# Kernel tuning notes

Measured on AMD Instinct MI355X. Metric: run time of the kernel, lower is better.

The kernel has to match this reference:

```python
import jax, jax.numpy as jnp
import numpy as np


def setup_inputs() -> dict:
    key = jax.random.key(0)
    k1, k2 = jax.random.split(key)
    sat = jax.random.normal(k1, (32, 64, 64, 64), dtype=jnp.float32)
    grd = jax.random.normal(k2, (32, 64, 64, 64), dtype=jnp.float32)
    return {"sat_features": sat, "grd_features": grd}


def _corr(sat, grd):
    # sat: [Bs,C,H,W], grd: [Bg,C,gh,gw] with H==gh and W==gw (enforced by source asserts)
    Bs, C, H, W = sat.shape
    Bg, _, gh, gw = grd.shape
    n = gw - 1
    # source circularly pads the HEIGHT axis by gw-1 (inner_warp_pad_columns, dim=2)
    satpad = jnp.concatenate([sat, sat[:, :, :n, :]], axis=2)  # [Bs,C,H+gw-1,W]
    # torch conv2d is cross-correlation with kernel = grd flipped along width.
    # Batch all Bs x Bg pairs as one conv: kernels are OIHW with O=Bg.
    kernel = jnp.flip(grd, axis=3)  # [Bg,C,gh,gw]
    out = jax.lax.conv_general_dilated(
        satpad, kernel, window_strides=(1, 1), padding='VALID',
        dimension_numbers=('NCHW', 'OIHW', 'NCHW'))  # [Bs,Bg,gw,1]
    out = out[..., 0]                                # [Bs,Bg,gw] (squeeze(3))
    orien = jnp.argmax(out, axis=2)                  # [Bs,Bg] int
    return out, orien


def _crop_sat(sat, orien, grd_width):
    # Per-pair circular shift along sat WIDTH, then crop first grd_width columns.
    Bs, C, H, W = sat.shape
    Bg = orien.shape[1]
    idx = (jnp.arange(grd_width)[None, None, :] + orien[:, :, None]) % W  # [Bs,Bg,gw]
    sat_e = jnp.broadcast_to(sat[:, None], (Bs, Bg, C, H, W))
    idx_e = jnp.broadcast_to(idx[:, :, None, None, :], (Bs, Bg, C, H, grd_width))
    # cropped[i,j,c,h,k] = sat[i,c,h,(k+orien[i,j]) % W]
    return jnp.take_along_axis(sat_e, idx_e, axis=4)  # [Bs,Bg,C,H,grd_width]


def _forward(sat, grd):
    corr_out, orien = _corr(sat, grd)
    grd_width = grd.shape[2]
    cropped = _crop_sat(sat, orien, grd_width)
    norm = jnp.sqrt(jnp.sum(cropped ** 2, axis=(2, 3, 4), keepdims=True) + 1e-8)
    sat_matrix = cropped / norm
    dot = jnp.sum(sat_matrix * grd[None], axis=(2, 3, 4))  # [Bs,Bg]
    distance = 2.0 - 2.0 * dot.T                           # [Bg,Bs]
    return distance, orien


def reference(sat_features, grd_features):
    distance, orien = _forward(sat_features, grd_features)
    return (sat_features, grd_features, distance, orien)
```

## Files before the change

### kernel.cpp

```cpp
#include <hip/hip_runtime.h>

typedef _Float16 f16;
typedef _Float16 f16x8 __attribute__((ext_vector_type(8)));
typedef float f32x16 __attribute__((ext_vector_type(16)));

#define SAT_ELEMS (32*64*64*64)
#define PER_I (64*64*64)
#define DIST_OFF (2*SAT_ELEMS)
#define ORIEN_OFF (DIST_OFF + 32*32)

#define WS_NORMS 0
#define WS_ORIEN 64
#define WS_CORR  2048
#define WS_DOTS  67584

__global__ __launch_bounds__(256) void zero_kernel(float* __restrict__ ws) {
  int t = blockIdx.x * 256 + threadIdx.x;
  if (t < 65536 + 1024) ws[WS_CORR + t] = 0.f;
}

__global__ __launch_bounds__(256) void copy_kernel(const float4* __restrict__ sat,
                                                   const float4* __restrict__ grd,
                                                   float4* __restrict__ out) {
  const int n4 = SAT_ELEMS / 4;
  int idx = blockIdx.x * 256 + threadIdx.x;
  int stride = gridDim.x * 256;
  for (int t = idx; t < n4; t += stride) out[t] = sat[t];
  for (int t = idx; t < n4; t += stride) out[n4 + t] = grd[t];
}

__global__ __launch_bounds__(256) void norm_kernel(const float4* __restrict__ sat,
                                                   float* __restrict__ norms) {
  int i = blockIdx.x;
  const float4* p = sat + (size_t)i * (PER_I / 4);
  float s = 0.f;
  for (int t = threadIdx.x; t < PER_I / 4; t += 256) {
    float4 v = p[t];
    s += v.x * v.x + v.y * v.y + v.z * v.z + v.w * v.w;
  }
  for (int off = 32; off; off >>= 1) s += __shfl_down(s, off, 64);
  __shared__ float red[4];
  int lane = threadIdx.x & 63, wv = threadIdx.x >> 6;
  if (lane == 0) red[wv] = s;
  __syncthreads();
  if (threadIdx.x == 0) norms[i] = sqrtf(red[0] + red[1] + red[2] + red[3] + 1e-8f);
}

__global__ __launch_bounds__(512) void gram3_kernel(const float* __restrict__ sat,
                                                    const float* __restrict__ grd,
                                                    float* __restrict__ ws) {
  __shared__ f16 As[2][256][64];
  __shared__ f16 Bs[2][128][64];
  __shared__ float corr_s[8][64];

  const int bid = blockIdx.x;
  const int ipg = bid & 7;
  const int rem = bid >> 3;
  const int jpg = rem >> 2;
  const int kz  = rem & 3;

  const int tid = threadIdx.x;
  const int lane = tid & 63;
  const int wv = tid >> 6;
  const int wr = wv >> 1, wc = wv & 1;
  const int lr = lane & 31, lh = lane >> 5;

  const int ra = tid >> 1, ua = tid & 1;
  const int ia = ipg * 4 + (ra >> 6), ha = ra & 63;
  const bool hasB = (tid < 256);
  const int rb = (tid >> 1) & 127, ub = tid & 1;
  const int jb = jpg * 2 + (rb >> 6), hb = rb & 63;

  const float* abase = sat + (size_t)ia * PER_I + (size_t)ha * 64;
  const float* bbase = grd + (size_t)jb * PER_I + (size_t)hb * 64;

  f32x16 acc[2][2];
  #pragma unroll
  for (int mh = 0; mh < 2; ++mh)
    #pragma unroll
    for (int nh = 0; nh < 2; ++nh)
      #pragma unroll
      for (int q = 0; q < 16; ++q) acc[mh][nh][q] = 0.f;

  float4 avA[4], avB[4];

  auto LOADA = [&](int S) {
    const int c = S >> 1, w0 = (S & 1) * 32;
    const float* p = abase + (size_t)c * 4096 + w0 + ua * 16;
    #pragma unroll
    for (int q = 0; q < 4; ++q) avA[q] = *(const float4*)(p + q * 4);
  };
  auto LOADB = [&](int S) {
    const int c = S >> 1, w0 = (S & 1) * 32;
    const float* p = bbase + (size_t)c * 4096;
    #pragma unroll
    for (int q = 0; q < 4; ++q) avB[q] = *(const float4*)(p + 60 - w0 - ub * 16 - q * 4);
  };
  auto WRITEA = [&](int buf) {
    f16* row = &As[buf][ra][0];
    const int rx = ra & 7;
    #pragma unroll
    for (int half = 0; half < 2; ++half) {
      f16x8 h, l;
      #pragma unroll
      for (int q = 0; q < 2; ++q) {
        float4 v = avA[half * 2 + q];
        const float xs[4] = {v.x, v.y, v.z, v.w};
        #pragma unroll
        for (int e = 0; e < 4; ++e) {
          f16 hh = (f16)xs[e];
          h[q * 4 + e] = hh;
          l[q * 4 + e] = (f16)(xs[e] - (float)hh);
        }
      }
      const int ck = 2 * ua + half;
      *(f16x8*)(row + ((ck ^ rx) * 8)) = h;
      *(f16x8*)(row + (((ck + 4) ^ rx) * 8)) = l;
    }
  };
  auto WRITEB = [&](int buf) {
    f16* row = &Bs[buf][rb][0];
    const int rx = rb & 7;
    #pragma unroll
    for (int half = 0; half < 2; ++half) {
      f16x8 h, l;
      #pragma unroll
      for (int q = 0; q < 2; ++q) {
        float4 v = avB[half * 2 + q];
        const float xs[4] = {v.w, v.z, v.y, v.x};
        #pragma unroll
        for (int e = 0; e < 4; ++e) {
          f16 hh = (f16)xs[e];
          h[q * 4 + e] = hh;
          l[q * 4 + e] = (f16)(xs[e] - (float)hh);
        }
      }
      const int ck = 2 * ub + half;
      *(f16x8*)(row + ((ck ^ rx) * 8)) = h;
      *(f16x8*)(row + (((ck + 4) ^ rx) * 8)) = l;
    }
  };

  const int aro = wr * 64, bro = wc * 64;
  const int S0 = kz * 32;

  LOADA(S0); if (hasB) LOADB(S0);
  WRITEA(0); if (hasB) WRITEB(0);
  __syncthreads();

  int cur = 0;
  for (int s = 0; s < 32; ++s) {
    if (s < 31) { LOADA(S0 + s + 1); if (hasB) LOADB(S0 + s + 1); }
    #pragma unroll
    for (int kk = 0; kk < 2; ++kk) {
      f16x8 ah[2], al[2], bh[2], bl[2];
      const int c0 = kk * 2 + lh;
      #pragma unroll
      for (int mh = 0; mh < 2; ++mh) {
        const int r1 = aro + mh * 32 + lr, rk1 = r1 & 7;
        ah[mh] = *(const f16x8*)(&As[cur][r1][0] + ((c0 ^ rk1) * 8));
        al[mh] = *(const f16x8*)(&As[cur][r1][0] + (((c0 + 4) ^ rk1) * 8));
        const int r2 = bro + mh * 32 + lr, rk2 = r2 & 7;
        bh[mh] = *(const f16x8*)(&Bs[cur][r2][0] + ((c0 ^ rk2) * 8));
        bl[mh] = *(const f16x8*)(&Bs[cur][r2][0] + (((c0 + 4) ^ rk2) * 8));
      }
      #pragma unroll
      for (int mh = 0; mh < 2; ++mh)
        #pragma unroll
        for (int nh = 0; nh < 2; ++nh) {
          acc[mh][nh] = __builtin_amdgcn_mfma_f32_32x32x16_f16(ah[mh], bh[nh], acc[mh][nh], 0, 0, 0);
          acc[mh][nh] = __builtin_amdgcn_mfma_f32_32x32x16_f16(ah[mh], bl[nh], acc[mh][nh], 0, 0, 0);
          acc[mh][nh] = __builtin_amdgcn_mfma_f32_32x32x16_f16(al[mh], bh[nh], acc[mh][nh], 0, 0, 0);
        }
    }
    if (s < 31) { WRITEA(cur ^ 1); if (hasB) WRITEB(cur ^ 1); }
    __syncthreads();
    cur ^= 1;
  }

  ((float*)corr_s)[tid] = 0.f;
  __syncthreads();
  const int p = wr * 2 + wc;
  #pragma unroll
  for (int r = 0; r < 16; ++r) {
    const int rowof = (r & 3) + 8 * (r >> 2);
    const int y0 = (rowof + 4 * lh - lr) & 63;
    const int y1 = (y0 + 32) & 63;
    atomicAdd(&corr_s[p][y0], acc[0][0][r] + acc[1][1][r]);
    atomicAdd(&corr_s[p][y1], acc[0][1][r] + acc[1][0][r]);
  }
  __syncthreads();
  {
    const int pp = tid >> 6, y = tid & 63;
    const int ip = ipg * 4 + (pp >> 1), jp = jpg * 2 + (pp & 1);
    atomicAdd(&ws[WS_CORR + ((size_t)ip * 32 + jp) * 64 + y], corr_s[pp][y]);
  }
}

__global__ __launch_bounds__(256) void argmax_kernel(const float* __restrict__ ws,
                                                     float* __restrict__ out,
                                                     int* __restrict__ orien) {
  int p = blockIdx.x * 256 + threadIdx.x;
  if (p >= 1024) return;
  const float* c = ws + WS_CORR + (size_t)p * 64;
  float best = c[0];
  int by = 0;
  for (int y = 1; y < 64; ++y) {
    float v = c[y];
    if (v > best) { best = v; by = y; }
  }
  orien[p] = by;
  out[ORIEN_OFF + p] = (float)by;
}

__global__ __launch_bounds__(512) void dot3_kernel(const float* __restrict__ sat,
                                                   const float* __restrict__ grd,
                                                   const int* __restrict__ orien,
                                                   float* __restrict__ dots) {
  const int bi = blockIdx.x;
  const int bj = blockIdx.y;
  const int bz = blockIdx.z;
  const int tid = threadIdx.x, lane = tid & 63, wvj = tid >> 6;
  const int j = bj * 8 + wvj;
  const int r0 = bz * 256;
  const int i0 = bi * 8;
  const float* gp = grd + (size_t)j * PER_I + (size_t)r0 * 64 + lane;
  const float* sp[8];
  #pragma unroll
  for (int q = 0; q < 8; ++q)
    sp[q] = sat + (size_t)(i0 + q) * PER_I + (size_t)r0 * 64
                + ((lane + orien[(i0 + q) * 32 + j]) & 63);
  float a[8] = {0.f, 0.f, 0.f, 0.f, 0.f, 0.f, 0.f, 0.f};
  #pragma unroll 2
  for (int r = 0; r < 256; ++r) {
    float g = gp[(size_t)r * 64];
    #pragma unroll
    for (int q = 0; q < 8; ++q) a[q] = fmaf(sp[q][(size_t)r * 64], g, a[q]);
  }
  #pragma unroll
  for (int q = 0; q < 8; ++q) {
    float s = a[q];
    for (int off = 32; off; off >>= 1) s += __shfl_down(s, off, 64);
    if (lane == 0) atomicAdd(&dots[(i0 + q) * 32 + j], s);
  }
}

__global__ __launch_bounds__(256) void finalize_kernel(const float* __restrict__ ws,
                                                       float* __restrict__ out) {
  int t = blockIdx.x * 256 + threadIdx.x;
  if (t >= 1024) return;
  int jj = t >> 5, ii = t & 31;
  float dot = ws[WS_DOTS + ii * 32 + jj] / ws[WS_NORMS + ii];
  out[DIST_OFF + jj * 32 + ii] = 2.f - 2.f * dot;
}

extern "C" void kernel_launch(void* const* d_in, const int* in_sizes, int n_in,
                              void* d_out, int out_size, void* d_ws, size_t ws_size,
                              hipStream_t stream) {
  const float* sat = (const float*)d_in[0];
  const float* grd = (const float*)d_in[1];
  float* out = (float*)d_out;
  float* wsf = (float*)d_ws;

  zero_kernel<<<260, 256, 0, stream>>>(wsf);
  copy_kernel<<<2048, 256, 0, stream>>>((const float4*)sat, (const float4*)grd, (float4*)out);
  norm_kernel<<<32, 256, 0, stream>>>((const float4*)sat, wsf + WS_NORMS);
  gram3_kernel<<<512, 512, 0, stream>>>(sat, grd, wsf);
  argmax_kernel<<<4, 256, 0, stream>>>(wsf, out, (int*)(wsf + WS_ORIEN));
  dot3_kernel<<<dim3(4, 4, 16), 512, 0, stream>>>(sat, grd, (const int*)(wsf + WS_ORIEN), wsf + WS_DOTS);
  finalize_kernel<<<4, 256, 0, stream>>>(wsf, out);
}
```

Before: 409.9 us.

## Pre-split inputs to fp16 hi/lo in workspace and stream via global_load_lds

Adds a split pass that converts sat and a width-flipped grd into fp16 high and low halves stored in workspace. A new correlation kernel with 256 threads, 128x128 tiles and K split in two loads these directly into LDS with global_load_lds, removing per-block fp32 loads and conversion. The dot-product kernel now reads only the fp16 high parts, halving its bytes at some precision cost. The new path runs only if the workspace is large enough, otherwise it falls back to the old kernels. The split pass adds a full extra read and write of both inputs.

```diff
diff --git a/kernel.cpp b/kernel.cpp
--- a/kernel.cpp
+++ b/kernel.cpp
@@ -1,4 +1,5 @@
 #include <hip/hip_runtime.h>
+#include <stdint.h>
 
 typedef _Float16 f16;
 typedef _Float16 f16x8 __attribute__((ext_vector_type(8)));
@@ -13,6 +14,17 @@
 #define WS_ORIEN 64
 #define WS_CORR  2048
 #define WS_DOTS  67584
+#define WSB_SATH (1u<<20)
+#define WSB_SATL (WSB_SATH + (uint32_t)SAT_ELEMS*2u)
+#define WSB_GRDH (WSB_SATL + (uint32_t)SAT_ELEMS*2u)
+#define WSB_GRDL (WSB_GRDH + (uint32_t)SAT_ELEMS*2u)
+#define WS_NEED  ((size_t)WSB_GRDL + (size_t)SAT_ELEMS*2u + 1024u)
+
+__device__ __forceinline__ void gll16(const void* src, void* dst) {
+  __builtin_amdgcn_global_load_lds(
+      (const __attribute__((address_space(1))) uint32_t*)src,
+      (__attribute__((address_space(3))) uint32_t*)dst, 16, 0, 0);
+}
 
 __global__ __launch_bounds__(256) void zero_kernel(float* __restrict__ ws) {
   int t = blockIdx.x * 256 + threadIdx.x;
@@ -46,33 +58,81 @@
   if (threadIdx.x == 0) norms[i] = sqrtf(red[0] + red[1] + red[2] + red[3] + 1e-8f);
 }
 
-__global__ __launch_bounds__(512) void gram3_kernel(const float* __restrict__ sat,
+__global__ __launch_bounds__(256) void split_kernel(const float* __restrict__ sat,
                                                     const float* __restrict__ grd,
-                                                    float* __restrict__ ws) {
-  __shared__ f16 As[2][256][64];
+                                                    uint8_t* __restrict__ wsb) {
+  f16* satH = (f16*)(wsb + WSB_SATH);
+  f16* satL = (f16*)(wsb + WSB_SATL);
+  f16* grdH = (f16*)(wsb + WSB_GRDH);
+  f16* grdL = (f16*)(wsb + WSB_GRDL);
+  const int NG = SAT_ELEMS / 8;
+  int idx = blockIdx.x * 256 + threadIdx.x;
+  int stride = gridDim.x * 256;
+  for (int g = idx; g < NG; g += stride) {
+    {
+      float4 f0 = *(const float4*)(sat + (size_t)g * 8);
+      float4 f1 = *(const float4*)(sat + (size_t)g * 8 + 4);
+      const float xs[8] = {f0.x, f0.y, f0.z, f0.w, f1.x, f1.y, f1.z, f1.w};
+      f16x8 h, l;
+      #pragma unroll
+      for (int e = 0; e < 8; ++e) {
+        f16 hh = (f16)xs[e];
+        h[e] = hh;
+        l[e] = (f16)(xs[e] - (float)hh);
+      }
+      *(f16x8*)(satH + (size_t)g * 8) = h;
+      *(f16x8*)(satL + (size_t)g * 8) = l;
+    }
+    {
+      int rowg = g >> 3, t = g & 7;
+      const float* gsrc = grd + (size_t)rowg * 64 + (56 - 8 * t);
+      float4 g0 = *(const float4*)(gsrc);
+      float4 g1 = *(const float4*)(gsrc + 4);
+      const float ys[8] = {g1.w, g1.z, g1.y, g1.x, g0.w, g0.z, g0.y, g0.x};
+      f16x8 h, l;
+      #pragma unroll
+      for (int e = 0; e < 8; ++e) {
+        f16 hh = (f16)ys[e];
+        h[e] = hh;
+        l[e] = (f16)(ys[e] - (float)hh);
+      }
+      *(f16x8*)(grdH + (size_t)g * 8) = h;
+      *(f16x8*)(grdL + (size_t)g * 8) = l;
+    }
+  }
+}
+
+__global__ __launch_bounds__(256, 2) void gram4_kernel(const uint8_t* __restrict__ wsb,
+                                                       float* __restrict__ ws) {
+  __shared__ f16 As[2][128][64];
   __shared__ f16 Bs[2][128][64];
-  __shared__ float corr_s[8][64];
+  __shared__ float corr_s[4][64];
 
   const int bid = blockIdx.x;
-  const int ipg = bid & 7;
-  const int rem = bid >> 3;
-  const int jpg = rem >> 2;
-  const int kz  = rem & 3;
-
-  const int tid = threadIdx.x;
-  const int lane = tid & 63;
-  const int wv = tid >> 6;
+  const int wg = (bid & 7) * 64 + (bid >> 3);
+  const int ipg = wg >> 5;
+  const int rem = wg & 31;
+  const int jpg = rem >> 1;
+  const int kz = rem & 1;
+
+  const int tid = threadIdx.x, lane = tid & 63, wv = tid >> 6;
   const int wr = wv >> 1, wc = wv & 1;
   const int lr = lane & 31, lh = lane >> 5;
 
-  const int ra = tid >> 1, ua = tid & 1;
-  const int ia = ipg * 4 + (ra >> 6), ha = ra & 63;
-  const bool hasB = (tid < 256);
-  const int rb = (tid >> 1) & 127, ub = tid & 1;
-  const int jb = jpg * 2 + (rb >> 6), hb = rb & 63;
-
-  const float* abase = sat + (size_t)ia * PER_I + (size_t)ha * 64;
-  const float* bbase = grd + (size_t)jb * PER_I + (size_t)hb * 64;
+  const int rsub = lane >> 3;
+  const int ck = (lane & 7) ^ rsub;
+  uint32_t aoff[4], boff[4];
+  #pragma unroll
+  for (int q = 0; q < 4; ++q) {
+    const int cc = wv * 4 + q;
+    const int row = cc * 8 + rsub;
+    const int h = row & 63, sub = row >> 6;
+    const uint32_t lanepart = 2u * ((uint32_t)h * 64u + (uint32_t)(ck & 3) * 8u);
+    aoff[q] = (ck < 4 ? WSB_SATH : WSB_SATL)
+            + 2u * (uint32_t)(ipg * 2 + sub) * (uint32_t)PER_I + lanepart;
+    boff[q] = (ck < 4 ? WSB_GRDH : WSB_GRDL)
+            + 2u * (uint32_t)(jpg * 2 + sub) * (uint32_t)PER_I + lanepart;
+  }
 
   f32x16 acc[2][2];
   #pragma unroll
@@ -82,85 +142,33 @@
       #pragma unroll
       for (int q = 0; q < 16; ++q) acc[mh][nh][q] = 0.f;
 
-  float4 avA[4], avB[4];
-
-  auto LOADA = [&](int S) {
-    const int c = S >> 1, w0 = (S & 1) * 32;
-    const float* p = abase + (size_t)c * 4096 + w0 + ua * 16;
-    #pragma unroll
-    for (int q = 0; q < 4; ++q) avA[q] = *(const float4*)(p + q * 4);
+  auto ISSUE = [&](int s, int buf) {
+    const int k0 = kz * 2048 + s * 32;
+    const uint32_t so = 2u * ((uint32_t)(k0 >> 6) * 4096u + (uint32_t)(k0 & 63));
+    #pragma unroll
+    for (int q = 0; q < 4; ++q) {
+      const int cc = wv * 4 + q;
+      gll16(wsb + aoff[q] + so, &As[buf][cc * 8][0]);
+      gll16(wsb + boff[q] + so, &Bs[buf][cc * 8][0]);
+    }
   };
-  auto LOADB = [&](int S) {
-    const int c = S >> 1, w0 = (S & 1) * 32;
-    const float* p = bbase + (size_t)c * 4096;
-    #pragma unroll
-    for (int q = 0; q < 4; ++q) avB[q] = *(const float4*)(p + 60 - w0 - ub * 16 - q * 4);
-  };
-  auto WRITEA = [&](int buf) {
-    f16* row = &As[buf][ra][0];
-    const int rx = ra & 7;
-    #pragma unroll
-    for (int half = 0; half < 2; ++half) {
-      f16x8 h, l;
-      #pragma unroll
-      for (int q = 0; q < 2; ++q) {
-        float4 v = avA[half * 2 + q];
-        const float xs[4] = {v.x, v.y, v.z, v.w};
-        #pragma unroll
-        for (int e = 0; e < 4; ++e) {
-          f16 hh = (f16)xs[e];
-          h[q * 4 + e] = hh;
-          l[q * 4 + e] = (f16)(xs[e] - (float)hh);
-        }
-      }
-      const int ck = 2 * ua + half;
-      *(f16x8*)(row + ((ck ^ rx) * 8)) = h;
-      *(f16x8*)(row + (((ck + 4) ^ rx) * 8)) = l;
-    }
-  };
-  auto WRITEB = [&](int buf) {
-    f16* row = &Bs[buf][rb][0];
-    const int rx = rb & 7;
-    #pragma unroll
-    for (int half = 0; half < 2; ++half) {
-      f16x8 h, l;
-      #pragma unroll
-      for (int q = 0; q < 2; ++q) {
-        float4 v = avB[half * 2 + q];
-        const float xs[4] = {v.w, v.z, v.y, v.x};
-        #pragma unroll
-        for (int e = 0; e < 4; ++e) {
-          f16 hh = (f16)xs[e];
-          h[q * 4 + e] = hh;
-          l[q * 4 + e] = (f16)(xs[e] - (float)hh);
-        }
-      }
-      const int ck = 2 * ub + half;
-      *(f16x8*)(row + ((ck ^ rx) * 8)) = h;
-      *(f16x8*)(row + (((ck + 4) ^ rx) * 8)) = l;
-    }
-  };
-
-  const int aro = wr * 64, bro = wc * 64;
-  const int S0 = kz * 32;
-
-  LOADA(S0); if (hasB) LOADB(S0);
-  WRITEA(0); if (hasB) WRITEB(0);
+
+  ISSUE(0, 0);
   __syncthreads();
 
   int cur = 0;
-  for (int s = 0; s < 32; ++s) {
-    if (s < 31) { LOADA(S0 + s + 1); if (hasB) LOADB(S0 + s + 1); }
+  for (int s = 0; s < 64; ++s) {
+    if (s < 63) ISSUE(s + 1, cur ^ 1);
     #pragma unroll
     for (int kk = 0; kk < 2; ++kk) {
       f16x8 ah[2], al[2], bh[2], bl[2];
       const int c0 = kk * 2 + lh;
       #pragma unroll
       for (int mh = 0; mh < 2; ++mh) {
-        const int r1 = aro + mh * 32 + lr, rk1 = r1 & 7;
+        const int r1 = wr * 64 + mh * 32 + lr, rk1 = r1 & 7;
         ah[mh] = *(const f16x8*)(&As[cur][r1][0] + ((c0 ^ rk1) * 8));
         al[mh] = *(const f16x8*)(&As[cur][r1][0] + (((c0 + 4) ^ rk1) * 8));
-        const int r2 = bro + mh * 32 + lr, rk2 = r2 & 7;
+        const int r2 = wc * 64 + mh * 32 + lr, rk2 = r2 & 7;
         bh[mh] = *(const f16x8*)(&Bs[cur][r2][0] + ((c0 ^ rk2) * 8));
         bl[mh] = *(const f16x8*)(&Bs[cur][r2][0] + (((c0 + 4) ^ rk2) * 8));
       }
@@ -173,26 +181,24 @@
           acc[mh][nh] = __builtin_amdgcn_mfma_f32_32x32x16_f16(al[mh], bh[nh], acc[mh][nh], 0, 0, 0);
         }
     }
-    if (s < 31) { WRITEA(cur ^ 1); if (hasB) WRITEB(cur ^ 1); }
     __syncthreads();
     cur ^= 1;
   }
 
-  ((float*)corr_s)[tid] = 0.f;
-  __syncthreads();
-  const int p = wr * 2 + wc;
+  if (tid < 256) ((float*)corr_s)[tid] = 0.f;
+  __syncthreads();
   #pragma unroll
   for (int r = 0; r < 16; ++r) {
     const int rowof = (r & 3) + 8 * (r >> 2);
     const int y0 = (rowof + 4 * lh - lr) & 63;
     const int y1 = (y0 + 32) & 63;
-    atomicAdd(&corr_s[p][y0], acc[0][0][r] + acc[1][1][r]);
-    atomicAdd(&corr_s[p][y1], acc[0][1][r] + acc[1][0][r]);
+    atomicAdd(&corr_s[wv][y0], acc[0][0][r] + acc[1][1][r]);
+    atomicAdd(&corr_s[wv][y1], acc[0][1][r] + acc[1][0][r]);
   }
   __syncthreads();
   {
     const int pp = tid >> 6, y = tid & 63;
-    const int ip = ipg * 4 + (pp >> 1), jp = jpg * 2 + (pp & 1);
+    const int ip = ipg * 2 + (pp >> 1), jp = jpg * 2 + (pp & 1);
     atomicAdd(&ws[WS_CORR + ((size_t)ip * 32 + jp) * 64 + y], corr_s[pp][y]);
   }
 }
@@ -211,6 +217,188 @@
   }
   orien[p] = by;
   out[ORIEN_OFF + p] = (float)by;
+}
+
+__global__ __launch_bounds__(512) void dot4_kernel(const uint8_t* __restrict__ wsb,
+                                                   const int* __restrict__ orien,
+                                                   float* __restrict__ dots) {
+  const f16* satH = (const f16*)(wsb + WSB_SATH);
+  const f16* grdH = (const f16*)(wsb + WSB_GRDH);
+  const int bi = blockIdx.x;
+  const int bj = blockIdx.y;
+  const int bz = blockIdx.z;
+  const int tid = threadIdx.x, lane = tid & 63, wvj = tid >> 6;
+  const int j = bj * 8 + wvj;
+  const int r0 = bz * 256;
+  const int i0 = bi * 8;
+  const f16* gp = grdH + (size_t)j * PER_I + (size_t)r0 * 64 + (63 - lane);
+  const f16* sp[8];
+  #pragma unroll
+  for (int q = 0; q < 8; ++q)
+    sp[q] = satH + (size_t)(i0 + q) * PER_I + (size_t)r0 * 64
+                 + ((lane + orien[(i0 + q) * 32 + j]) & 63);
+  float a[8] = {0.f, 0.f, 0.f, 0.f, 0.f, 0.f, 0.f, 0.f};
+  #pragma unroll 2
+  for (int r = 0; r < 256; ++r) {
+    float g = (float)gp[(size_t)r * 64];
+    #pragma unroll
+    for (int q = 0; q < 8; ++q) a[q] = fmaf((float)sp[q][(size_t)r * 64], g, a[q]);
+  }
+  #pragma unroll
+  for (int q = 0; q < 8; ++q) {
+    float s = a[q];
+    for (int off = 32; off; off >>= 1) s += __shfl_down(s, off, 64);
+    if (lane == 0) atomicAdd(&dots[(i0 + q) * 32 + j], s);
+  }
+}
+
+__global__ __launch_bounds__(256) void finalize_kernel(const float* __restrict__ ws,
+                                                       float* __restrict__ out) {
+  int t = blockIdx.x * 256 + threadIdx.x;
+  if (t >= 1024) return;
+  int jj = t >> 5, ii = t & 31;
+  float dot = ws[WS_DOTS + ii * 32 + jj] / ws[WS_NORMS + ii];
+  out[DIST_OFF + jj * 32 + ii] = 2.f - 2.f * dot;
+}
+
+__global__ __launch_bounds__(512) void gram3_kernel(const float* __restrict__ sat,
+                                                    const float* __restrict__ grd,
+                                                    float* __restrict__ ws) {
+  __shared__ f16 As[2][256][64];
+  __shared__ f16 Bs[2][128][64];
+  __shared__ float corr_s[8][64];
+  const int bid = blockIdx.x;
+  const int ipg = bid & 7;
+  const int rem = bid >> 3;
+  const int jpg = rem >> 2;
+  const int kz  = rem & 3;
+  const int tid = threadIdx.x;
+  const int lane = tid & 63;
+  const int wv = tid >> 6;
+  const int wr = wv >> 1, wc = wv & 1;
+  const int lr = lane & 31, lh = lane >> 5;
+  const int ra = tid >> 1, ua = tid & 1;
+  const int ia = ipg * 4 + (ra >> 6), ha = ra & 63;
+  const bool hasB = (tid < 256);
+  const int rb = (tid >> 1) & 127, ub = tid & 1;
+  const int jb = jpg * 2 + (rb >> 6), hb = rb & 63;
+  const float* abase = sat + (size_t)ia * PER_I + (size_t)ha * 64;
+  const float* bbase = grd + (size_t)jb * PER_I + (size_t)hb * 64;
+  f32x16 acc[2][2];
+  #pragma unroll
+  for (int mh = 0; mh < 2; ++mh)
+    #pragma unroll
+    for (int nh = 0; nh < 2; ++nh)
+      #pragma unroll
+      for (int q = 0; q < 16; ++q) acc[mh][nh][q] = 0.f;
+  float4 avA[4], avB[4];
+  auto LOADA = [&](int S) {
+    const int c = S >> 1, w0 = (S & 1) * 32;
+    const float* p = abase + (size_t)c * 4096 + w0 + ua * 16;
+    #pragma unroll
+    for (int q = 0; q < 4; ++q) avA[q] = *(const float4*)(p + q * 4);
+  };
+  auto LOADB = [&](int S) {
+    const int c = S >> 1, w0 = (S & 1) * 32;
+    const float* p = bbase + (size_t)c * 4096;
+    #pragma unroll
+    for (int q = 0; q < 4; ++q) avB[q] = *(const float4*)(p + 60 - w0 - ub * 16 - q * 4);
+  };
+  auto WRITEA = [&](int buf) {
+    f16* row = &As[buf][ra][0];
+    const int rx = ra & 7;
+    #pragma unroll
+    for (int half = 0; half < 2; ++half) {
+      f16x8 h, l;
+      #pragma unroll
+      for (int q = 0; q < 2; ++q) {
+        float4 v = avA[half * 2 + q];
+        const float xs[4] = {v.x, v.y, v.z, v.w};
+        #pragma unroll
+        for (int e = 0; e < 4; ++e) {
+          f16 hh = (f16)xs[e];
+          h[q * 4 + e] = hh;
+          l[q * 4 + e] = (f16)(xs[e] - (float)hh);
+        }
+      }
+      const int ckk = 2 * ua + half;
+      *(f16x8*)(row + ((ckk ^ rx) * 8)) = h;
+      *(f16x8*)(row + (((ckk + 4) ^ rx) * 8)) = l;
+    }
+  };
+  auto WRITEB = [&](int buf) {
+    f16* row = &Bs[buf][rb][0];
+    const int rx = rb & 7;
+    #pragma unroll
+    for (int half = 0; half < 2; ++half) {
+      f16x8 h, l;
+      #pragma unroll
+      for (int q = 0; q < 2; ++q) {
+        float4 v = avB[half * 2 + q];
+        const float xs[4] = {v.w, v.z, v.y, v.x};
+        #pragma unroll
+        for (int e = 0; e < 4; ++e) {
+          f16 hh = (f16)xs[e];
+          h[q * 4 + e] = hh;
+          l[q * 4 + e] = (f16)(xs[e] - (float)hh);
+        }
+      }
+      const int ckk = 2 * ub + half;
+      *(f16x8*)(row + ((ckk ^ rx) * 8)) = h;
+      *(f16x8*)(row + (((ckk + 4) ^ rx) * 8)) = l;
+    }
+  };
+  const int aro = wr * 64, bro = wc * 64;
+  const int S0 = kz * 32;
+  LOADA(S0); if (hasB) LOADB(S0);
+  WRITEA(0); if (hasB) WRITEB(0);
+  __syncthreads();
+  int cur = 0;
+  for (int s = 0; s < 32; ++s) {
+    if (s < 31) { LOADA(S0 + s + 1); if (hasB) LOADB(S0 + s + 1); }
+    #pragma unroll
+    for (int kk = 0; kk < 2; ++kk) {
+      f16x8 ah[2], al[2], bh[2], bl[2];
+      const int c0 = kk * 2 + lh;
+      #pragma unroll
+      for (int mh = 0; mh < 2; ++mh) {
+        const int r1 = aro + mh * 32 + lr, rk1 = r1 & 7;
+        ah[mh] = *(const f16x8*)(&As[cur][r1][0] + ((c0 ^ rk1) * 8));
+        al[mh] = *(const f16x8*)(&As[cur][r1][0] + (((c0 + 4) ^ rk1) * 8));
+        const int r2 = bro + mh * 32 + lr, rk2 = r2 & 7;
+        bh[mh] = *(const f16x8*)(&Bs[cur][r2][0] + ((c0 ^ rk2) * 8));
+        bl[mh] = *(const f16x8*)(&Bs[cur][r2][0] + (((c0 + 4) ^ rk2) * 8));
+      }
+      #pragma unroll
+      for (int mh = 0; mh < 2; ++mh)
+        #pragma unroll
+        for (int nh = 0; nh < 2; ++nh) {
+          acc[mh][nh] = __builtin_amdgcn_mfma_f32_32x32x16_f16(ah[mh], bh[nh], acc[mh][nh], 0, 0, 0);
+          acc[mh][nh] = __builtin_amdgcn_mfma_f32_32x32x16_f16(ah[mh], bl[nh], acc[mh][nh], 0, 0, 0);
+          acc[mh][nh] = __builtin_amdgcn_mfma_f32_32x32x16_f16(al[mh], bh[nh], acc[mh][nh], 0, 0, 0);
+        }
+    }
+    if (s < 31) { WRITEA(cur ^ 1); if (hasB) WRITEB(cur ^ 1); }
+    __syncthreads();
+    cur ^= 1;
+  }
+  ((float*)corr_s)[tid] = 0.f;
+  __syncthreads();
+  const int p = wr * 2 + wc;
+  #pragma unroll
+  for (int r = 0; r < 16; ++r) {
+    const int rowof = (r & 3) + 8 * (r >> 2);
+    const int y0 = (rowof + 4 * lh - lr) & 63;
+    const int y1 = (y0 + 32) & 63;
+    atomicAdd(&corr_s[p][y0], acc[0][0][r] + acc[1][1][r]);
+    atomicAdd(&corr_s[p][y1], acc[0][1][r] + acc[1][0][r]);
+  }
+  __syncthreads();
+  {
+    const int pp = tid >> 6, y = tid & 63;
+    const int ip = ipg * 4 + (pp >> 1), jp = jpg * 2 + (pp & 1);
+    atomicAdd(&ws[WS_CORR + ((size_t)ip * 32 + jp) * 64 + y], corr_s[pp][y]);
+  }
 }
 
 __global__ __launch_bounds__(512) void dot3_kernel(const float* __restrict__ sat,
@@ -245,15 +433,6 @@
   }
 }
 
-__global__ __launch_bounds__(256) void finalize_kernel(const float* __restrict__ ws,
-                                                       float* __restrict__ out) {
-  int t = blockIdx.x * 256 + threadIdx.x;
-  if (t >= 1024) return;
-  int jj = t >> 5, ii = t & 31;
-  float dot = ws[WS_DOTS + ii * 32 + jj] / ws[WS_NORMS + ii];
-  out[DIST_OFF + jj * 32 + ii] = 2.f - 2.f * dot;
-}
-
 extern "C" void kernel_launch(void* const* d_in, const int* in_sizes, int n_in,
                               void* d_out, int out_size, void* d_ws, size_t ws_size,
                               hipStream_t stream) {
@@ -261,12 +440,21 @@
   const float* grd = (const float*)d_in[1];
   float* out = (float*)d_out;
   float* wsf = (float*)d_ws;
+  uint8_t* wsb = (uint8_t*)d_ws;
 
   zero_kernel<<<260, 256, 0, stream>>>(wsf);
   copy_kernel<<<2048, 256, 0, stream>>>((const float4*)sat, (const float4*)grd, (float4*)out);
   norm_kernel<<<32, 256, 0, stream>>>((const float4*)sat, wsf + WS_NORMS);
-  gram3_kernel<<<512, 512, 0, stream>>>(sat, grd, wsf);
-  argmax_kernel<<<4, 256, 0, stream>>>(wsf, out, (int*)(wsf + WS_ORIEN));
-  dot3_kernel<<<dim3(4, 4, 16), 512, 0, stream>>>(sat, grd, (const int*)(wsf + WS_ORIEN), wsf + WS_DOTS);
+
+  if (ws_size >= WS_NEED) {
+    split_kernel<<<2048, 256, 0, stream>>>(sat, grd, wsb);
+    gram4_kernel<<<512, 256, 0, stream>>>(wsb, wsf);
+    argmax_kernel<<<4, 256, 0, stream>>>(wsf, out, (int*)(wsf + WS_ORIEN));
+    dot4_kernel<<<dim3(4, 4, 16), 512, 0, stream>>>(wsb, (const int*)(wsf + WS_ORIEN), wsf + WS_DOTS);
+  } else {
+    gram3_kernel<<<512, 512, 0, stream>>>(sat, grd, wsf);
+    argmax_kernel<<<4, 256, 0, stream>>>(wsf, out, (int*)(wsf + WS_ORIEN));
+    dot3_kernel<<<dim3(4, 4, 16), 512, 0, stream>>>(sat, grd, (const int*)(wsf + WS_ORIEN), wsf + WS_DOTS);
+  }
   finalize_kernel<<<4, 256, 0, stream>>>(wsf, out);
 }
```

After: 404.2 us. About the same (-1.4%).
